# Optimization experiments

Measured on AMD Instinct MI355X. Metric: run time of the kernel, lower is better.

Reference implementation:

```python
import jax, jax.numpy as jnp
import numpy as np

B, D, H, C = 8192, 2048, 4096, 64
HALF = D // 2
BLOCKS = 2


def setup_inputs() -> dict:
    key = jax.random.key(0)
    ks = jax.random.split(key, 8)
    z = jax.random.normal(ks[0], (B, D), jnp.float32)
    condition = jax.random.normal(ks[1], (B, C), jnp.float32)
    # alternating masks: block 0 identity=odd indices, transform=even; block 1 flipped
    even = jnp.arange(0, D, 2, dtype=jnp.int32)
    odd = jnp.arange(1, D, 2, dtype=jnp.int32)
    idx_id = jnp.stack([odd, even])   # [BLOCKS, HALF]
    idx_tr = jnp.stack([even, odd])   # [BLOCKS, HALF]
    def init_w(k, shape, fan_in):
        return jax.random.normal(k, shape, jnp.float32) * np.float32(1.0 / np.sqrt(fan_in))
    W1 = init_w(ks[2], (BLOCKS, HALF + C, H), HALF + C)
    b1 = jnp.zeros((BLOCKS, H), jnp.float32)
    W2 = init_w(ks[3], (BLOCKS, H, H), H)
    b2 = jnp.zeros((BLOCKS, H), jnp.float32)
    W3 = init_w(ks[4], (BLOCKS, H, 2 * HALF), H) * np.float32(0.01)  # keep exp(S) tame
    b3 = jnp.zeros((BLOCKS, 2 * HALF), jnp.float32)
    return {"z": z, "condition": condition, "idx_id": idx_id, "idx_tr": idx_tr,
            "W1": W1, "b1": b1, "W2": W2, "b2": b2, "W3": W3, "b3": b3}


def reference(z, condition, idx_id, idx_tr, W1, b1, W2, b2, W3, b3):
    # F_zx of the affine coupling layer (scale_tanh=False, clamp_scale=None)
    x = z
    log_det = jnp.zeros((z.shape[0], 1), z.dtype)
    for i in range(BLOCKS):
        # gather identity channels, condition on external vector
        h = jnp.concatenate([x[:, idx_id[i]], condition], axis=-1)  # [B, HALF+C]
        h = jax.nn.relu(h @ W1[i] + b1[i])
        h = jax.nn.relu(h @ W2[i] + b2[i])
        out = (h @ W3[i] + b3[i]).reshape(x.shape[0], HALF, 2)
        S = out[..., 0]  # scale logits
        T = out[..., 1]  # translation
        # scatter-update transformed channels
        x = x.at[:, idx_tr[i]].set(x[:, idx_tr[i]] * jnp.exp(S) + T)
        log_det = log_det + jnp.sum(S, axis=1, keepdims=True)
    return x, log_det
```

## Files before the change

kernel.cpp:

```cpp
#include <hip/hip_runtime.h>
#include <hip/hip_bf16.h>

#define B_    8192
#define D_    2048
#define H_    4096
#define C_    64
#define HALF_ 1024
#define KIN_  1088

typedef __attribute__((ext_vector_type(8))) short bf16x8;
typedef __attribute__((ext_vector_type(4))) float f32x4;

__device__ __forceinline__ unsigned short f2bf(float f) {
  __hip_bfloat16 h = __float2bfloat16(f);
  return *reinterpret_cast<unsigned short*>(&h);
}

__device__ __forceinline__ void gload16(const void* g, void* s) {
  __builtin_amdgcn_global_load_lds((const __attribute__((address_space(1))) void*)g,
                                   (__attribute__((address_space(3))) void*)s,
                                   16, 0, 0);
}

__global__ void convT(const float* __restrict__ W, unsigned short* __restrict__ Wt,
                      int K, int N) {
  __shared__ float tile[32][33];
  int tx = threadIdx.x & 31, ty = threadIdx.x >> 5;
  int n0 = blockIdx.x * 32, k0 = blockIdx.y * 32;
#pragma unroll
  for (int i = 0; i < 4; ++i)
    tile[ty + i * 8][tx] = W[(size_t)(k0 + ty + i * 8) * N + n0 + tx];
  __syncthreads();
#pragma unroll
  for (int i = 0; i < 4; ++i)
    Wt[(size_t)(n0 + ty + i * 8) * K + k0 + tx] = f2bf(tile[tx][ty + i * 8]);
}

__global__ void build_act(const float* __restrict__ xsrc, const float* __restrict__ cond,
                          int par, unsigned short* __restrict__ A0) {
  int row = blockIdx.y;
  int col = blockIdx.x * 256 + threadIdx.x;
  if (col >= KIN_) return;
  float v;
  if (col < HALF_) {
    float2 p = ((const float2*)xsrc)[(size_t)row * (D_ / 2) + col];
    v = par ? p.y : p.x;
  } else {
    v = cond[(size_t)row * C_ + (col - HALF_)];
  }
  A0[(size_t)row * KIN_ + col] = f2bf(v);
}

template <int MODE>
__global__ __launch_bounds__(1024, 4)
void gemmk(const unsigned short* __restrict__ A,
           const unsigned short* __restrict__ Bt,
           const float* __restrict__ bias,
           unsigned short* __restrict__ Cout,
           const float* __restrict__ xold, float* __restrict__ xnew,
           float* __restrict__ part, int par,
           int M, int N, int K) {
  __shared__ unsigned short lds[65536];
  char* ldsb = (char*)lds;
  const int tid = threadIdx.x;
  const int w = tid >> 6, lane = tid & 63;
  const int fr = lane & 15, fq = lane >> 4;
  const int wr = w >> 2, wc = w & 3;

  const int nbx = N >> 8;
  const int nwg = (int)gridDim.x;
  const int cpx = nwg >> 3;
  const int bid = (int)blockIdx.x;
  const int swz = (bid & 7) * cpx + (bid >> 3);
  const int by = swz / nbx, bx = swz - by * nbx;
  const int m0 = by << 8, n0 = bx << 8;

  const int chunkp = (((fr & 1) << 2) | fq) ^ (fr >> 1);
  const int A0 = (wr * 32 + (fr >> 1)) * 128 + chunkp * 16;
  const int B0 = 16384 + (wc * 32 + (fr >> 1)) * 128 + chunkp * 16;

  const int q = tid;
  const int p = q >> 3, cph = q & 7;
  const int clg = cph ^ (p & 7);
  const int rowS = 2 * p + (clg >> 2);
  const int kcolS = (clg & 3) * 8;
  const unsigned short* sA0 = A + (size_t)(m0 + rowS) * K + kcolS;
  const unsigned short* sB0 = Bt + (size_t)(n0 + rowS) * K + kcolS;
  const int dst0 = tid * 16;

#define STAGE_ALL(OFF) do {                                                  \
    gload16(sA0, ldsb + (OFF) + dst0);                                       \
    gload16(sB0, ldsb + (OFF) + 16384 + dst0);                               \
    sA0 += 32; sB0 += 32;                                                    \
  } while (0)

#define WIN(STG, VM)                                                         \
  {                                                                          \
    __builtin_amdgcn_s_barrier();                                            \
    __builtin_amdgcn_sched_barrier(0);                                       \
    bf16x8 av[4], bv[4];                                                     \
    _Pragma("unroll") for (int n = 0; n < 4; ++n)                            \
      bv[n] = *(const bf16x8*)(ldsb + cur + B0 + n * 1024);                  \
    _Pragma("unroll") for (int m = 0; m < 4; ++m)                            \
      av[m] = *(const bf16x8*)(ldsb + cur + A0 + m * 1024);                  \
    if (STG) STAGE_ALL(stg);                                                 \
    __builtin_amdgcn_s_setprio(1);                                           \
    _Pragma("unroll") for (int m = 0; m < 4; ++m)                            \
      _Pragma("unroll") for (int n = 0; n < 4; ++n)                          \
        acc[m][n] = __builtin_amdgcn_mfma_f32_16x16x32_bf16(                 \
            av[m], bv[n], acc[m][n], 0, 0, 0);                               \
    __builtin_amdgcn_s_setprio(0);                                           \
    if (VM == 1) asm volatile("s_waitcnt vmcnt(2)" ::: "memory");            \
    if (VM == 2) asm volatile("s_waitcnt vmcnt(0)" ::: "memory");            \
    __builtin_amdgcn_sched_barrier(0);                                       \
    cur = (cur == 65536) ? 0 : cur + 32768;                                  \
    stg = (stg == 65536) ? 0 : stg + 32768;                                  \
  }

  f32x4 acc[4][4];
  f32x4 z4 = {0.f, 0.f, 0.f, 0.f};
#pragma unroll
  for (int m = 0; m < 4; ++m)
#pragma unroll
    for (int n = 0; n < 4; ++n) acc[m][n] = z4;

  const int NT = K >> 5;

  STAGE_ALL(0);
  STAGE_ALL(32768);
  asm volatile("s_waitcnt vmcnt(2)" ::: "memory");
  __builtin_amdgcn_sched_barrier(0);
  int cur = 0, stg = 65536;

  for (int T = 0; T < NT - 2; ++T) {
    WIN(1, 1)
  }
  WIN(0, 2)
  WIN(0, 0)
#undef WIN
#undef STAGE_ALL

  if (MODE == 0) {
    __builtin_amdgcn_s_barrier();
#pragma unroll
    for (int m = 0; m < 4; ++m)
#pragma unroll
      for (int n = 0; n < 4; ++n) {
        int gcol = n0 + wc * 64 + n * 16 + fr;
        float bb = bias[gcol];
#pragma unroll
        for (int r = 0; r < 4; ++r) {
          float v = fmaxf(acc[m][n][r] + bb, 0.f);
          int lrow = m * 16 + fq * 4 + r;
          *(unsigned short*)(ldsb + w * 8192 + lrow * 128 + ((n ^ fq) * 32) + fr * 2) = f2bf(v);
        }
      }
    asm volatile("s_waitcnt lgkmcnt(0)" ::: "memory");
    __builtin_amdgcn_sched_barrier(0);
    unsigned short* Cb = Cout + (size_t)(m0 + wr * 64) * N + n0 + wc * 64;
    const int sub = lane & 7;
#pragma unroll
    for (int i = 0; i < 8; ++i) {
      int lrow = i * 8 + (lane >> 3);
      int phys = (sub >> 1) ^ ((lrow >> 2) & 3);
      bf16x8 val = *(const bf16x8*)(ldsb + w * 8192 + lrow * 128 + phys * 32 + (sub & 1) * 16);
      *(bf16x8*)(Cb + (size_t)lrow * N + sub * 8) = val;
    }
  } else {
#pragma unroll
    for (int m = 0; m < 4; ++m) {
      float srow[4] = {0.f, 0.f, 0.f, 0.f};
#pragma unroll
      for (int n = 0; n < 4; ++n) {
        int gcol = n0 + wc * 64 + n * 16 + fr;
        float bb = bias[gcol];
#pragma unroll
        for (int r = 0; r < 4; ++r) {
          float v = acc[m][n][r] + bb;
          float vp = __shfl_xor(v, 1);
          if (!(fr & 1)) {
            int grow = m0 + wr * 64 + m * 16 + fq * 4 + r;
            size_t idx = (size_t)grow * N + gcol + par;
            xnew[idx] = xold[idx] * expf(v) + vp;
            srow[r] += v;
          }
        }
      }
#pragma unroll
      for (int r = 0; r < 4; ++r) {
        float s = srow[r];
        s += __shfl_xor(s, 2);
        s += __shfl_xor(s, 4);
        s += __shfl_xor(s, 8);
        if (fr == 0) {
          int grow = m0 + wr * 64 + m * 16 + fq * 4 + r;
          part[(size_t)grow * 32 + bx * 4 + wc] = s;
        }
      }
    }
  }
}

__global__ void reduce_logdet(const float* __restrict__ P, float* __restrict__ logdet, int add) {
  int row = blockIdx.x * 256 + threadIdx.x;
  float s = 0.f;
#pragma unroll
  for (int g = 0; g < 32; ++g) s += P[(size_t)row * 32 + g];
  logdet[row] = add ? (logdet[row] + s) : s;
}

extern "C" void kernel_launch(void* const* d_in, const int* in_sizes, int n_in,
                              void* d_out, int out_size, void* d_ws, size_t ws_size,
                              hipStream_t stream) {
  const float* z    = (const float*)d_in[0];
  const float* cond = (const float*)d_in[1];
  const float* W1   = (const float*)d_in[4];
  const float* b1   = (const float*)d_in[5];
  const float* W2   = (const float*)d_in[6];
  const float* b2   = (const float*)d_in[7];
  const float* W3   = (const float*)d_in[8];
  const float* b3   = (const float*)d_in[9];

  float* xout   = (float*)d_out;
  float* logdet = xout + (size_t)B_ * D_;

  char* ws = (char*)d_ws;
  unsigned short* Wt = (unsigned short*)ws;
  unsigned short* H1 = (unsigned short*)(ws + 33554432);
  unsigned short* H2 = (unsigned short*)(ws + 33554432 + 67108864);
  float* Pp = (float*)H1;
  unsigned short* A0 = H2;

  for (int blk = 0; blk < 2; ++blk) {
    const float* W1b = W1 + (size_t)blk * KIN_ * H_;
    const float* W2b = W2 + (size_t)blk * H_ * H_;
    const float* W3b = W3 + (size_t)blk * H_ * D_;
    const float* b1b = b1 + (size_t)blk * H_;
    const float* b2b = b2 + (size_t)blk * H_;
    const float* b3b = b3 + (size_t)blk * D_;
    const float* xsrc = blk ? xout : z;

    convT<<<dim3(H_ / 32, KIN_ / 32), 256, 0, stream>>>(W1b, Wt, KIN_, H_);
    build_act<<<dim3(5, B_), 256, 0, stream>>>(xsrc, cond, 1 - blk, A0);
    gemmk<0><<<dim3((B_ / 256) * (H_ / 256)), 1024, 0, stream>>>(
        A0, Wt, b1b, H1, nullptr, nullptr, nullptr, 0, B_, H_, KIN_);

    convT<<<dim3(H_ / 32, H_ / 32), 256, 0, stream>>>(W2b, Wt, H_, H_);
    gemmk<0><<<dim3((B_ / 256) * (H_ / 256)), 1024, 0, stream>>>(
        H1, Wt, b2b, H2, nullptr, nullptr, nullptr, 0, B_, H_, H_);

    convT<<<dim3(D_ / 32, H_ / 32), 256, 0, stream>>>(W3b, Wt, H_, D_);
    gemmk<1><<<dim3((B_ / 256) * (D_ / 256)), 1024, 0, stream>>>(
        H2, Wt, b3b, nullptr, z, xout, Pp, blk, B_, D_, H_);

    reduce_logdet<<<dim3(B_ / 256), 256, 0, stream>>>(Pp, logdet, blk);
  }
}
```

Before: 991.5 us.

## Prepack weights into MFMA fragment order and load B directly to registers

The weight transpose kernel now writes bf16 weights in a packed layout that matches the per-lane MFMA B-fragment order. The GEMM reads each B fragment straight from global memory into registers with one 16-byte load per fragment, so only A is staged in LDS. The LDS buffers shrink and the barrier moves to the end of each K step. The intent is to cut LDS traffic and staging for B. In exchange, B loads sit on the critical path without LDS reuse across the waves that share a column, and each wave waits on global latency every iteration.

```diff
diff --git a/kernel.cpp b/kernel.cpp
--- a/kernel.cpp
+++ b/kernel.cpp
@@ -22,8 +22,8 @@
                                    16, 0, 0);
 }
 
-__global__ void convT(const float* __restrict__ W, unsigned short* __restrict__ Wt,
-                      int K, int N) {
+__global__ void convT_pack(const float* __restrict__ W, unsigned short* __restrict__ Bp,
+                           int K, int N) {
   __shared__ float tile[32][33];
   int tx = threadIdx.x & 31, ty = threadIdx.x >> 5;
   int n0 = blockIdx.x * 32, k0 = blockIdx.y * 32;
@@ -31,9 +31,17 @@
   for (int i = 0; i < 4; ++i)
     tile[ty + i * 8][tx] = W[(size_t)(k0 + ty + i * 8) * N + n0 + tx];
   __syncthreads();
-#pragma unroll
-  for (int i = 0; i < 4; ++i)
-    Wt[(size_t)(n0 + ty + i * 8) * K + k0 + tx] = f2bf(tile[tx][ty + i * 8]);
+  int lane = threadIdx.x & 63;
+  int fr = lane & 15, fq = lane >> 4;
+  int cl = (threadIdx.x >> 6) & 1;
+  int eh = threadIdx.x >> 7;
+  int cn = (n0 >> 4) + cl, ck = k0 >> 5;
+  unsigned short out[4];
+#pragma unroll
+  for (int e2 = 0; e2 < 4; ++e2)
+    out[e2] = f2bf(tile[fq * 8 + eh * 4 + e2][cl * 16 + fr]);
+  size_t base = ((size_t)(cn * (K >> 5) + ck) * 64 + lane) * 8 + eh * 4;
+  *(ushort4*)(Bp + base) = *(ushort4*)out;
 }
 
 __global__ void build_act(const float* __restrict__ xsrc, const float* __restrict__ cond,
@@ -54,7 +62,7 @@
 template <int MODE>
 __global__ __launch_bounds__(1024, 4)
 void gemmk(const unsigned short* __restrict__ A,
-           const unsigned short* __restrict__ Bt,
+           const unsigned short* __restrict__ Bp,
            const float* __restrict__ bias,
            unsigned short* __restrict__ Cout,
            const float* __restrict__ xold, float* __restrict__ xnew,
@@ -77,44 +85,50 @@
 
   const int chunkp = (((fr & 1) << 2) | fq) ^ (fr >> 1);
   const int A0 = (wr * 32 + (fr >> 1)) * 128 + chunkp * 16;
-  const int B0 = 16384 + (wc * 32 + (fr >> 1)) * 128 + chunkp * 16;
-
-  const int q = tid;
-  const int p = q >> 3, cph = q & 7;
+
+  const int p = tid >> 3, cph = tid & 7;
   const int clg = cph ^ (p & 7);
   const int rowS = 2 * p + (clg >> 2);
   const int kcolS = (clg & 3) * 8;
   const unsigned short* sA0 = A + (size_t)(m0 + rowS) * K + kcolS;
-  const unsigned short* sB0 = Bt + (size_t)(n0 + rowS) * K + kcolS;
   const int dst0 = tid * 16;
 
-#define STAGE_ALL(OFF) do {                                                  \
+  const int NTK = K >> 5;
+  const int cn0 = (n0 >> 4) + wc * 4;
+  const unsigned short* pB0 = Bp + ((size_t)(cn0 + 0) * NTK * 64 + lane) * 8;
+  const unsigned short* pB1 = Bp + ((size_t)(cn0 + 1) * NTK * 64 + lane) * 8;
+  const unsigned short* pB2 = Bp + ((size_t)(cn0 + 2) * NTK * 64 + lane) * 8;
+  const unsigned short* pB3 = Bp + ((size_t)(cn0 + 3) * NTK * 64 + lane) * 8;
+
+#define STAGE_A(OFF) do {                                                    \
     gload16(sA0, ldsb + (OFF) + dst0);                                       \
-    gload16(sB0, ldsb + (OFF) + 16384 + dst0);                               \
-    sA0 += 32; sB0 += 32;                                                    \
+    sA0 += 32;                                                               \
   } while (0)
 
 #define WIN(STG, VM)                                                         \
   {                                                                          \
-    __builtin_amdgcn_s_barrier();                                            \
-    __builtin_amdgcn_sched_barrier(0);                                       \
     bf16x8 av[4], bv[4];                                                     \
-    _Pragma("unroll") for (int n = 0; n < 4; ++n)                            \
-      bv[n] = *(const bf16x8*)(ldsb + cur + B0 + n * 1024);                  \
+    bv[0] = *(const bf16x8*)pB0; pB0 += 512;                                 \
+    bv[1] = *(const bf16x8*)pB1; pB1 += 512;                                 \
+    bv[2] = *(const bf16x8*)pB2; pB2 += 512;                                 \
+    bv[3] = *(const bf16x8*)pB3; pB3 += 512;                                 \
     _Pragma("unroll") for (int m = 0; m < 4; ++m)                            \
       av[m] = *(const bf16x8*)(ldsb + cur + A0 + m * 1024);                  \
-    if (STG) STAGE_ALL(stg);                                                 \
+    if (STG) STAGE_A(stg);                                                   \
+    __builtin_amdgcn_sched_barrier(0);                                       \
     __builtin_amdgcn_s_setprio(1);                                           \
     _Pragma("unroll") for (int m = 0; m < 4; ++m)                            \
       _Pragma("unroll") for (int n = 0; n < 4; ++n)                          \
         acc[m][n] = __builtin_amdgcn_mfma_f32_16x16x32_bf16(                 \
             av[m], bv[n], acc[m][n], 0, 0, 0);                               \
     __builtin_amdgcn_s_setprio(0);                                           \
-    if (VM == 1) asm volatile("s_waitcnt vmcnt(2)" ::: "memory");            \
+    __builtin_amdgcn_sched_barrier(0);                                       \
+    if (VM == 1) asm volatile("s_waitcnt vmcnt(1)" ::: "memory");            \
     if (VM == 2) asm volatile("s_waitcnt vmcnt(0)" ::: "memory");            \
     __builtin_amdgcn_sched_barrier(0);                                       \
-    cur = (cur == 65536) ? 0 : cur + 32768;                                  \
-    stg = (stg == 65536) ? 0 : stg + 32768;                                  \
+    __builtin_amdgcn_s_barrier();                                            \
+    cur = (cur == 32768) ? 0 : cur + 16384;                                  \
+    stg = (stg == 32768) ? 0 : stg + 16384;                                  \
   }
 
   f32x4 acc[4][4];
@@ -126,11 +140,12 @@
 
   const int NT = K >> 5;
 
-  STAGE_ALL(0);
-  STAGE_ALL(32768);
-  asm volatile("s_waitcnt vmcnt(2)" ::: "memory");
+  STAGE_A(0);
+  STAGE_A(16384);
+  asm volatile("s_waitcnt vmcnt(1)" ::: "memory");
   __builtin_amdgcn_sched_barrier(0);
-  int cur = 0, stg = 65536;
+  __builtin_amdgcn_s_barrier();
+  int cur = 0, stg = 32768;
 
   for (int T = 0; T < NT - 2; ++T) {
     WIN(1, 1)
@@ -138,7 +153,7 @@
   WIN(0, 2)
   WIN(0, 0)
 #undef WIN
-#undef STAGE_ALL
+#undef STAGE_A
 
   if (MODE == 0) {
     __builtin_amdgcn_s_barrier();
@@ -240,16 +255,16 @@
     const float* b3b = b3 + (size_t)blk * D_;
     const float* xsrc = blk ? xout : z;
 
-    convT<<<dim3(H_ / 32, KIN_ / 32), 256, 0, stream>>>(W1b, Wt, KIN_, H_);
+    convT_pack<<<dim3(H_ / 32, KIN_ / 32), 256, 0, stream>>>(W1b, Wt, KIN_, H_);
     build_act<<<dim3(5, B_), 256, 0, stream>>>(xsrc, cond, 1 - blk, A0);
     gemmk<0><<<dim3((B_ / 256) * (H_ / 256)), 1024, 0, stream>>>(
         A0, Wt, b1b, H1, nullptr, nullptr, nullptr, 0, B_, H_, KIN_);
 
-    convT<<<dim3(H_ / 32, H_ / 32), 256, 0, stream>>>(W2b, Wt, H_, H_);
+    convT_pack<<<dim3(H_ / 32, H_ / 32), 256, 0, stream>>>(W2b, Wt, H_, H_);
     gemmk<0><<<dim3((B_ / 256) * (H_ / 256)), 1024, 0, stream>>>(
         H1, Wt, b2b, H2, nullptr, nullptr, nullptr, 0, B_, H_, H_);
 
-    convT<<<dim3(D_ / 32, H_ / 32), 256, 0, stream>>>(W3b, Wt, H_, D_);
+    convT_pack<<<dim3(D_ / 32, H_ / 32), 256, 0, stream>>>(W3b, Wt, H_, D_);
     gemmk<1><<<dim3((B_ / 256) * (D_ / 256)), 1024, 0, stream>>>(
         H2, Wt, b3b, nullptr, z, xout, Pp, blk, B_, D_, H_);
 
```

New measurement: 1.318 ms. 33.0% more time.
